# Kernel optimization log

Hardware: AMD Instinct MI355X
Metric: run time of the kernel (lower is better)

Reference implementation:

```python
import jax, jax.numpy as jnp
import numpy as np

N_STATE = 1024
N_HEAD = 16
HEAD_DIM = N_STATE // N_HEAD


def setup_inputs() -> dict:
    key = jax.random.key(0)
    ks = jax.random.split(key, 8)
    s = 0.02
    return {
        "x": jax.random.normal(ks[0], (4, 1500, N_STATE), dtype=jnp.float32),
        "Wq": jax.random.normal(ks[1], (N_STATE, N_STATE), dtype=jnp.float32) * s,
        "bq": jnp.zeros((N_STATE,), dtype=jnp.float32),
        "Wk": jax.random.normal(ks[2], (N_STATE, N_STATE), dtype=jnp.float32) * s,
        "Wv": jax.random.normal(ks[3], (N_STATE, N_STATE), dtype=jnp.float32) * s,
        "bv": jnp.zeros((N_STATE,), dtype=jnp.float32),
        "Wo": jax.random.normal(ks[4], (N_STATE, N_STATE), dtype=jnp.float32) * s,
        "bo": jnp.zeros((N_STATE,), dtype=jnp.float32),
    }


def reference(x, Wq, bq, Wk, Wv, bv, Wo, bo):
    B, S, _ = x.shape
    scale = HEAD_DIM ** (-0.5)
    # projections (torch Linear: y = x @ W.T + b)
    q = x @ Wq.T + bq
    k = x @ Wk.T
    v = x @ Wv.T + bv
    # [B, H, S, D]
    q = q.reshape(B, S, N_HEAD, HEAD_DIM).transpose(0, 2, 1, 3)
    k = k.reshape(B, S, N_HEAD, HEAD_DIM).transpose(0, 2, 1, 3)
    v = v.reshape(B, S, N_HEAD, HEAD_DIM).transpose(0, 2, 1, 3)
    # scores scaled AFTER the matmul, as in the original (qk * qk_scale)
    qk = jnp.einsum("bhqd,bhkd->bhqk", q, k) * scale
    w = jax.nn.softmax(qk, axis=-1)
    wv = jnp.einsum("bhqk,bhkd->bhqd", w, v)
    wv = wv.transpose(0, 2, 1, 3).reshape(B, S, N_STATE)
    return wv @ Wo.T + bo
```

## Files before the change

### kernel.cpp

```cpp
#include <hip/hip_runtime.h>
#include <hip/hip_bf16.h>
#include <stdint.h>

#define S_LEN  1500
#define S_PAD  1536
#define BATCH  4
#define NSTATE 1024
#define NHEAD  16
#define HDIM   64
#define MROWS  6000
#define C1     0.180336879f

typedef __attribute__((ext_vector_type(8)))  short short8;
typedef __attribute__((ext_vector_type(4)))  float floatx4;
typedef __attribute__((ext_vector_type(16))) float floatx16;

__device__ __forceinline__ unsigned short f2bf(float f) {
  union { float f; unsigned int u; } v; v.f = f;
  unsigned int r = v.u + 0x7fffu + ((v.u >> 16) & 1u);
  return (unsigned short)(r >> 16);
}

__device__ __forceinline__ void gld_lds16(const void* g, void* l) {
  __builtin_amdgcn_global_load_lds(
      (const __attribute__((address_space(1))) void*)g,
      (__attribute__((address_space(3))) void*)l, 16, 0, 0);
}

__global__ __launch_bounds__(256) void cvt_all(
    const float* __restrict__ x,  const float* __restrict__ Wq,
    const float* __restrict__ Wk, const float* __restrict__ Wv,
    const float* __restrict__ Wo, unsigned short* __restrict__ dst)
{
  const size_t NX = (size_t)MROWS * NSTATE;
  size_t e = ((size_t)blockIdx.x * 256 + threadIdx.x) * 4;
  const float* src; size_t off;
  if (e < NX) { src = x; off = e; }
  else {
    size_t t = e - NX;
    int wsel = (int)(t >> 20);
    off = t & ((1u << 20) - 1);
    src = (wsel == 0) ? Wq : (wsel == 1) ? Wk : (wsel == 2) ? Wv : Wo;
  }
  float4 v = *(const float4*)(src + off);
  uint2 o;
  o.x = (unsigned int)f2bf(v.x) | ((unsigned int)f2bf(v.y) << 16);
  o.y = (unsigned int)f2bf(v.z) | ((unsigned int)f2bf(v.w) << 16);
  *(uint2*)(dst + e) = o;
}

template <bool F32OUT>
__device__ __forceinline__ void gemm128_bt(
    const unsigned short* __restrict__ X,
    const unsigned short* __restrict__ W,
    const float* __restrict__ bias,
    void* __restrict__ Yv,
    int m0, int n0, float scale)
{
  __shared__ unsigned short As[2][128 * 32];
  __shared__ unsigned short Bs[2][128 * 32];

  const int tid  = threadIdx.x;
  const int lane = tid & 63;
  const int wid  = tid >> 6;
  const int wm   = (wid & 1) * 64;
  const int wn   = (wid >> 1) * 64;
  const int l15  = lane & 15;
  const int l4   = lane >> 4;

  floatx4 acc[4][4];
#pragma unroll
  for (int i = 0; i < 4; ++i)
#pragma unroll
    for (int j = 0; j < 4; ++j)
      acc[i][j] = (floatx4){0.f, 0.f, 0.f, 0.f};

  const int srow  = tid >> 2;
  const int scolb = (tid & 3) * 16;

  const char* xrp[2];
  const char* wrp[2];
#pragma unroll
  for (int r = 0; r < 2; ++r) {
    int arow = m0 + r * 64 + srow;
    if (arow > MROWS - 1) arow = MROWS - 1;
    xrp[r] = (const char*)X + (size_t)arow * NSTATE * 2 + scolb;
    int brow = n0 + r * 64 + srow;
    wrp[r] = (const char*)W + (size_t)brow * NSTATE * 2 + scolb;
  }

  for (int k0 = 0; k0 < NSTATE; k0 += 64) {
    __syncthreads();
#pragma unroll
    for (int h = 0; h < 2; ++h) {
      int kb = (k0 + h * 32) * 2;
#pragma unroll
      for (int r = 0; r < 2; ++r) {
        gld_lds16(xrp[r] + kb, (char*)As[h] + r * 4096 + wid * 1024);
        gld_lds16(wrp[r] + kb, (char*)Bs[h] + r * 4096 + wid * 1024);
      }
    }
    __syncthreads();

#pragma unroll
    for (int h = 0; h < 2; ++h) {
      short8 a[4], b[4];
#pragma unroll
      for (int i = 0; i < 4; ++i)
        a[i] = *(const short8*)(As[h] + (wm + i * 16 + l15) * 32 + l4 * 8);
#pragma unroll
      for (int j = 0; j < 4; ++j)
        b[j] = *(const short8*)(Bs[h] + (wn + j * 16 + l15) * 32 + l4 * 8);
#pragma unroll
      for (int i = 0; i < 4; ++i)
#pragma unroll
        for (int j = 0; j < 4; ++j)
          acc[i][j] = __builtin_amdgcn_mfma_f32_16x16x32_bf16(a[i], b[j], acc[i][j], 0, 0, 0);
    }
  }

#pragma unroll
  for (int j = 0; j < 4; ++j) {
    int ng = n0 + wn + j * 16 + l15;
    float bias_v = bias ? bias[ng] : 0.f;
#pragma unroll
    for (int i = 0; i < 4; ++i) {
      int mgb = m0 + wm + i * 16 + l4 * 4;
#pragma unroll
      for (int r = 0; r < 4; ++r) {
        int mg = mgb + r;
        if (mg < MROWS) {
          float val = (acc[i][j][r] + bias_v) * scale;
          if (F32OUT) ((float*)Yv)[(size_t)mg * NSTATE + ng] = val;
          else        ((unsigned short*)Yv)[(size_t)mg * NSTATE + ng] = f2bf(val);
        }
      }
    }
  }
}

__global__ __launch_bounds__(256) void proj_qkv(
    const unsigned short* __restrict__ X,
    const unsigned short* __restrict__ Wq, const unsigned short* __restrict__ Wk,
    const unsigned short* __restrict__ Wv,
    const float* __restrict__ bq, const float* __restrict__ bv,
    unsigned short* __restrict__ q, unsigned short* __restrict__ k,
    unsigned short* __restrict__ v)
{
  const int z = blockIdx.z;
  const unsigned short* W = (z == 0) ? Wq : (z == 1) ? Wk : Wv;
  const float* bias       = (z == 0) ? bq : (z == 1) ? (const float*)nullptr : bv;
  unsigned short* Y       = (z == 0) ? q  : (z == 1) ? k  : v;
  float scale             = (z == 0) ? C1 : 1.0f;
  gemm128_bt<false>(X, W, bias, Y, blockIdx.y * 128, blockIdx.x * 128, scale);
}

__global__ __launch_bounds__(256) void proj_o(
    const unsigned short* __restrict__ X, const unsigned short* __restrict__ W,
    const float* __restrict__ bias, float* __restrict__ Y)
{
  gemm128_bt<true>(X, W, bias, Y, blockIdx.y * 128, blockIdx.x * 128, 1.0f);
}

__global__ __launch_bounds__(256) void vtrans(
    const unsigned short* __restrict__ v, unsigned short* __restrict__ vt)
{
  __shared__ unsigned short T[64][72];
  const int tid = threadIdx.x;
  const int st = blockIdx.x * 64, h = blockIdx.y, b = blockIdx.z;
#pragma unroll
  for (int rr = 0; rr < 2; ++rr) {
    int sl = rr * 32 + (tid >> 3);
    int dl = (tid & 7) * 8;
    int s  = st + sl;
    uint4 val = make_uint4(0u, 0u, 0u, 0u);
    if (s < S_LEN)
      val = *(const uint4*)&v[((size_t)b * S_LEN + s) * NSTATE + h * HDIM + dl];
    *(uint4*)&T[sl][dl] = val;
  }
  __syncthreads();
#pragma unroll
  for (int rr = 0; rr < 2; ++rr) {
    int dl = rr * 32 + (tid >> 3);
    int s0 = (tid & 7) * 8;
    unsigned short tmp[8];
#pragma unroll
    for (int j2 = 0; j2 < 8; ++j2) tmp[j2] = T[s0 + j2][dl];
    *(uint4*)&vt[(((size_t)b * NHEAD + h) * HDIM + dl) * S_PAD + st + s0] =
        *(const uint4*)tmp;
  }
}

__global__ __launch_bounds__(256, 4) void attn32t(
    const unsigned short* __restrict__ Q, const unsigned short* __restrict__ K,
    const unsigned short* __restrict__ VT, unsigned short* __restrict__ O)
{
  __shared__ unsigned short SMEM[16384];
  unsigned short* Ks  = SMEM;
  unsigned short* Vts = SMEM + 8192;
  unsigned short* Os  = SMEM;

  const int tid  = threadIdx.x;
  const int lane = tid & 63;
  const int w    = tid >> 6;
  const int l31  = lane & 31;
  const int lhi  = lane >> 5;
  const int qt = blockIdx.x, h = blockIdx.y, b = blockIdx.z;
  const size_t base  = ((size_t)b * S_LEN) * NSTATE + h * HDIM;
  const size_t vbase = (((size_t)b * NHEAD + h) * HDIM) * S_PAD;

  short8 qf[4];
  {
    int qrow = qt * 128 + w * 32 + l31;
    if (qrow > S_LEN - 1) qrow = S_LEN - 1;
    const unsigned short* qp = Q + base + (size_t)qrow * NSTATE;
#pragma unroll
    for (int c = 0; c < 4; ++c)
      qf[c] = *(const short8*)(qp + c * 16 + lhi * 8);
  }

  short8 ones;
#pragma unroll
  for (int i = 0; i < 8; ++i) ones[i] = (short)0x3F80;

  floatx16 oacc[2], oacc_l;
  oacc[0] = (floatx16)(0.f);
  oacc[1] = (floatx16)(0.f);
  oacc_l  = (floatx16)(0.f);

  for (int t = 0; t < 12; ++t) {
    __syncthreads();
#pragma unroll
    for (int qq = 0; qq < 4; ++qq) {
      int row  = (w * 4 + qq) * 8 + (lane >> 3);
      int logc = (lane & 7) ^ (row & 7);
      int s = t * 128 + row; if (s > S_LEN - 1) s = S_LEN - 1;
      gld_lds16(&K[base + (size_t)s * NSTATE + logc * 8],
                (char*)Ks + (w * 4 + qq) * 1024);
    }
#pragma unroll
    for (int qq = 0; qq < 4; ++qq) {
      int d    = (w * 4 + qq) * 4 + (lane >> 4);
      int logc = (lane & 15) ^ (d & 7);
      gld_lds16(&VT[vbase + (size_t)d * S_PAD + t * 128 + logc * 8],
                (char*)Vts + (w * 4 + qq) * 1024);
    }
    __syncthreads();

#pragma unroll
    for (int kvt = 0; kvt < 4; ++kvt) {
      floatx16 sacc = (floatx16)(0.f);
#pragma unroll
      for (int c = 0; c < 4; ++c) {
        int row  = kvt * 32 + l31;
        int phys = (c * 2 + lhi) ^ (row & 7);
        short8 ak = *(const short8*)(Ks + row * 64 + phys * 8);
        sacc = __builtin_amdgcn_mfma_f32_32x32x16_bf16(ak, qf[c], sacc, 0, 0, 0);
      }

      if (t == 11 && kvt >= 2) {
        if (kvt == 3) {
#pragma unroll
          for (int r = 0; r < 16; ++r) sacc[r] = -3.0e38f;
        } else {
#pragma unroll
          for (int r = 12; r < 16; ++r) sacc[r] = lhi ? -3.0e38f : sacc[r];
        }
      }

      unsigned int pk[8], ex[8];
#pragma unroll
      for (int i = 0; i < 8; ++i) {
        float p0 = exp2f(sacc[2 * i]);
        float p1 = exp2f(sacc[2 * i + 1]);
        __hip_bfloat162 h2 = __float22bfloat162_rn(float2{p0, p1});
        unsigned int u;
        __builtin_memcpy(&u, &h2, 4);
        pk[i] = u;
      }
#pragma unroll
      for (int i = 0; i < 8; ++i)
        ex[i] = __shfl_xor((unsigned int)pk[i], 32, 64);

      int4 f0i, f1i;
      f0i.x = lhi ? ex[2] : pk[0];
      f0i.y = lhi ? ex[3] : pk[1];
      f0i.z = lhi ? pk[2] : ex[0];
      f0i.w = lhi ? pk[3] : ex[1];
      f1i.x = lhi ? ex[6] : pk[4];
      f1i.y = lhi ? ex[7] : pk[5];
      f1i.z = lhi ? pk[6] : ex[4];
      f1i.w = lhi ? pk[7] : ex[5];
      short8 f0 = *(short8*)&f0i;
      short8 f1 = *(short8*)&f1i;

      oacc_l = __builtin_amdgcn_mfma_f32_32x32x16_bf16(ones, f0, oacc_l, 0, 0, 0);
      oacc_l = __builtin_amdgcn_mfma_f32_32x32x16_bf16(ones, f1, oacc_l, 0, 0, 0);

#pragma unroll
      for (int dt = 0; dt < 2; ++dt) {
        int d = dt * 32 + l31;
        int p0 = ((kvt * 4 + 0) + lhi) ^ (d & 7);
        int p1 = ((kvt * 4 + 2) + lhi) ^ (d & 7);
        short8 av0 = *(const short8*)(Vts + d * 128 + p0 * 8);
        short8 av1 = *(const short8*)(Vts + d * 128 + p1 * 8);
        oacc[dt] = __builtin_amdgcn_mfma_f32_32x32x16_bf16(av0, f0, oacc[dt], 0, 0, 0);
        oacc[dt] = __builtin_amdgcn_mfma_f32_32x32x16_bf16(av1, f1, oacc[dt], 0, 0, 0);
      }
    }
  }

  float inv = 1.f / oacc_l[0];

  __syncthreads();
#pragma unroll
  for (int dt = 0; dt < 2; ++dt)
#pragma unroll
    for (int g = 0; g < 4; ++g) {
      int d0 = dt * 32 + g * 8 + lhi * 4;
      float v0 = oacc[dt][4 * g + 0] * inv;
      float v1 = oacc[dt][4 * g + 1] * inv;
      float v2 = oacc[dt][4 * g + 2] * inv;
      float v3 = oacc[dt][4 * g + 3] * inv;
      uint2 pk2;
      pk2.x = (unsigned int)f2bf(v0) | ((unsigned int)f2bf(v1) << 16);
      pk2.y = (unsigned int)f2bf(v2) | ((unsigned int)f2bf(v3) << 16);
      *(uint2*)&Os[(w * 32 + l31) * 72 + d0] = pk2;
    }
  __syncthreads();
#pragma unroll
  for (int pass = 0; pass < 4; ++pass) {
    int e = pass * 256 + tid;
    int row = e >> 3, ch = e & 7;
    int s = qt * 128 + row;
    if (s < S_LEN)
      *(uint4*)&O[base + (size_t)s * NSTATE + ch * 8] = *(const uint4*)&Os[row * 72 + ch * 8];
  }
}

extern "C" void kernel_launch(void* const* d_in, const int* in_sizes, int n_in,
                              void* d_out, int out_size, void* d_ws, size_t ws_size,
                              hipStream_t stream) {
  const float* x  = (const float*)d_in[0];
  const float* Wq = (const float*)d_in[1];
  const float* bq = (const float*)d_in[2];
  const float* Wk = (const float*)d_in[3];
  const float* Wv = (const float*)d_in[4];
  const float* bv = (const float*)d_in[5];
  const float* Wo = (const float*)d_in[6];
  const float* bo = (const float*)d_in[7];
  float* out = (float*)d_out;

  const size_t NX = (size_t)MROWS * NSTATE;
  const size_t NW = (size_t)NSTATE * NSTATE;

  unsigned short* xb  = (unsigned short*)d_ws;
  unsigned short* Wqb = xb  + NX;
  unsigned short* Wkb = Wqb + NW;
  unsigned short* Wvb = Wkb + NW;
  unsigned short* Wob = Wvb + NW;
  unsigned short* q   = Wob + NW;
  unsigned short* k   = q + NX;
  unsigned short* v   = k + NX;
  unsigned short* vt  = v + NX;
  unsigned short* wv  = xb;

  dim3 blk(256);
  const size_t n4_total = (NX + 4 * NW) / 4;
  cvt_all<<<dim3((int)(n4_total / 256)), blk, 0, stream>>>(x, Wq, Wk, Wv, Wo, xb);
  proj_qkv<<<dim3(8, 47, 3), blk, 0, stream>>>(xb, Wqb, Wkb, Wvb, bq, bv, q, k, v);
  vtrans<<<dim3(24, NHEAD, BATCH), blk, 0, stream>>>(v, vt);
  attn32t<<<dim3(12, NHEAD, BATCH), blk, 0, stream>>>(q, k, vt, wv);
  proj_o<<<dim3(8, 47, 1), blk, 0, stream>>>(wv, Wob, bo, out);
}
```

Before: 284.3 us.

## Fuse V transpose into V-projection epilogue and swap GEMM grid order

The V projection now writes its output directly in the transposed, padded per-head layout through a shared-memory staged epilogue, removing the separate vtrans kernel and the intermediate V buffer round trip. The GEMM grids are also reoriented so blockIdx.x walks M tiles, changing block rasterization and cache reuse of weights. The padded tail columns of vt are no longer zero-filled, and the new epilogue adds an extra sync and division-based index math.

```diff
diff --git a/kernel.cpp b/kernel.cpp
--- a/kernel.cpp
+++ b/kernel.cpp
@@ -49,7 +49,7 @@
   *(uint2*)(dst + e) = o;
 }
 
-template <bool F32OUT>
+template <int MODE>
 __device__ __forceinline__ void gemm128_bt(
     const unsigned short* __restrict__ X,
     const unsigned short* __restrict__ W,
@@ -57,8 +57,9 @@
     void* __restrict__ Yv,
     int m0, int n0, float scale)
 {
-  __shared__ unsigned short As[2][128 * 32];
-  __shared__ unsigned short Bs[2][128 * 32];
+  __shared__ unsigned short SM[17408];
+  unsigned short* Asp = SM;
+  unsigned short* Bsp = SM + 8192;
 
   const int tid  = threadIdx.x;
   const int lane = tid & 63;
@@ -96,21 +97,23 @@
       int kb = (k0 + h * 32) * 2;
 #pragma unroll
       for (int r = 0; r < 2; ++r) {
-        gld_lds16(xrp[r] + kb, (char*)As[h] + r * 4096 + wid * 1024);
-        gld_lds16(wrp[r] + kb, (char*)Bs[h] + r * 4096 + wid * 1024);
+        gld_lds16(xrp[r] + kb, (char*)SM + h * 8192 + r * 4096 + wid * 1024);
+        gld_lds16(wrp[r] + kb, (char*)SM + 16384 + h * 8192 + r * 4096 + wid * 1024);
       }
     }
     __syncthreads();
 
 #pragma unroll
     for (int h = 0; h < 2; ++h) {
+      const unsigned short* Ah = Asp + h * 4096;
+      const unsigned short* Bh = Bsp + h * 4096;
       short8 a[4], b[4];
 #pragma unroll
       for (int i = 0; i < 4; ++i)
-        a[i] = *(const short8*)(As[h] + (wm + i * 16 + l15) * 32 + l4 * 8);
+        a[i] = *(const short8*)(Ah + (wm + i * 16 + l15) * 32 + l4 * 8);
 #pragma unroll
       for (int j = 0; j < 4; ++j)
-        b[j] = *(const short8*)(Bs[h] + (wn + j * 16 + l15) * 32 + l4 * 8);
+        b[j] = *(const short8*)(Bh + (wn + j * 16 + l15) * 32 + l4 * 8);
 #pragma unroll
       for (int i = 0; i < 4; ++i)
 #pragma unroll
@@ -119,20 +122,64 @@
     }
   }
 
-#pragma unroll
-  for (int j = 0; j < 4; ++j) {
-    int ng = n0 + wn + j * 16 + l15;
-    float bias_v = bias ? bias[ng] : 0.f;
-#pragma unroll
-    for (int i = 0; i < 4; ++i) {
-      int mgb = m0 + wm + i * 16 + l4 * 4;
-#pragma unroll
-      for (int r = 0; r < 4; ++r) {
-        int mg = mgb + r;
-        if (mg < MROWS) {
-          float val = (acc[i][j][r] + bias_v) * scale;
-          if (F32OUT) ((float*)Yv)[(size_t)mg * NSTATE + ng] = val;
-          else        ((unsigned short*)Yv)[(size_t)mg * NSTATE + ng] = f2bf(val);
+  if (MODE != 2) {
+#pragma unroll
+    for (int j = 0; j < 4; ++j) {
+      int ng = n0 + wn + j * 16 + l15;
+      float bias_v = bias ? bias[ng] : 0.f;
+#pragma unroll
+      for (int i = 0; i < 4; ++i) {
+        int mgb = m0 + wm + i * 16 + l4 * 4;
+#pragma unroll
+        for (int r = 0; r < 4; ++r) {
+          int mg = mgb + r;
+          if (mg < MROWS) {
+            float val = (acc[i][j][r] + bias_v) * scale;
+            if (MODE == 1) ((float*)Yv)[(size_t)mg * NSTATE + ng] = val;
+            else           ((unsigned short*)Yv)[(size_t)mg * NSTATE + ng] = f2bf(val);
+          }
+        }
+      }
+    }
+  } else {
+    unsigned short* vt = (unsigned short*)Yv;
+    __syncthreads();
+#pragma unroll
+    for (int j = 0; j < 4; ++j) {
+      int nl = wn + j * 16 + l15;
+      float bias_v = bias[n0 + nl];
+#pragma unroll
+      for (int i = 0; i < 4; ++i) {
+        int mlb = wm + i * 16 + l4 * 4;
+#pragma unroll
+        for (int r = 0; r < 4; ++r)
+          SM[nl * 136 + mlb + r] = f2bf(acc[i][j][r] + bias_v);
+      }
+    }
+    __syncthreads();
+#pragma unroll
+    for (int pass = 0; pass < 8; ++pass) {
+      int e   = pass * 256 + tid;
+      int nl  = e >> 4;
+      int m0l = (e & 15) * 8;
+      int ng  = n0 + nl;
+      int hh  = ng >> 6, dd = ng & 63;
+      int mg  = m0 + m0l;
+      int b1  = mg / 1500;
+      int s1  = mg - b1 * 1500;
+      if (mg + 7 < MROWS && s1 + 7 < S_LEN) {
+        *(uint4*)&vt[(((size_t)b1 * NHEAD + hh) * HDIM + dd) * S_PAD + s1] =
+            *(const uint4*)&SM[nl * 136 + m0l];
+      } else {
+#pragma unroll
+        for (int jj = 0; jj < 8; ++jj) {
+          int m = mg + jj;
+          if (m < MROWS) {
+            int b2 = m / 1500;
+            int s2 = m - b2 * 1500;
+            vt[(((size_t)b2 * NHEAD + hh) * HDIM + dd) * S_PAD + s2] =
+                SM[nl * 136 + m0l + jj];
+          }
         }
       }
     }
@@ -145,50 +192,20 @@
     const unsigned short* __restrict__ Wv,
     const float* __restrict__ bq, const float* __restrict__ bv,
     unsigned short* __restrict__ q, unsigned short* __restrict__ k,
-    unsigned short* __restrict__ v)
+    unsigned short* __restrict__ vt)
 {
   const int z = blockIdx.z;
-  const unsigned short* W = (z == 0) ? Wq : (z == 1) ? Wk : Wv;
-  const float* bias       = (z == 0) ? bq : (z == 1) ? (const float*)nullptr : bv;
-  unsigned short* Y       = (z == 0) ? q  : (z == 1) ? k  : v;
-  float scale             = (z == 0) ? C1 : 1.0f;
-  gemm128_bt<false>(X, W, bias, Y, blockIdx.y * 128, blockIdx.x * 128, scale);
+  const int m0 = blockIdx.x * 128, n0 = blockIdx.y * 128;
+  if (z == 0)      gemm128_bt<0>(X, Wq, bq,      q,  m0, n0, C1);
+  else if (z == 1) gemm128_bt<0>(X, Wk, nullptr, k,  m0, n0, 1.0f);
+  else             gemm128_bt<2>(X, Wv, bv,      vt, m0, n0, 1.0f);
 }
 
 __global__ __launch_bounds__(256) void proj_o(
     const unsigned short* __restrict__ X, const unsigned short* __restrict__ W,
     const float* __restrict__ bias, float* __restrict__ Y)
 {
-  gemm128_bt<true>(X, W, bias, Y, blockIdx.y * 128, blockIdx.x * 128, 1.0f);
-}
-
-__global__ __launch_bounds__(256) void vtrans(
-    const unsigned short* __restrict__ v, unsigned short* __restrict__ vt)
-{
-  __shared__ unsigned short T[64][72];
-  const int tid = threadIdx.x;
-  const int st = blockIdx.x * 64, h = blockIdx.y, b = blockIdx.z;
-#pragma unroll
-  for (int rr = 0; rr < 2; ++rr) {
-    int sl = rr * 32 + (tid >> 3);
-    int dl = (tid & 7) * 8;
-    int s  = st + sl;
-    uint4 val = make_uint4(0u, 0u, 0u, 0u);
-    if (s < S_LEN)
-      val = *(const uint4*)&v[((size_t)b * S_LEN + s) * NSTATE + h * HDIM + dl];
-    *(uint4*)&T[sl][dl] = val;
-  }
-  __syncthreads();
-#pragma unroll
-  for (int rr = 0; rr < 2; ++rr) {
-    int dl = rr * 32 + (tid >> 3);
-    int s0 = (tid & 7) * 8;
-    unsigned short tmp[8];
-#pragma unroll
-    for (int j2 = 0; j2 < 8; ++j2) tmp[j2] = T[s0 + j2][dl];
-    *(uint4*)&vt[(((size_t)b * NHEAD + h) * HDIM + dl) * S_PAD + st + s0] =
-        *(const uint4*)tmp;
-  }
+  gemm128_bt<1>(X, W, bias, Y, blockIdx.x * 128, blockIdx.y * 128, 1.0f);
 }
 
 __global__ __launch_bounds__(256, 4) void attn32t(
@@ -361,15 +378,13 @@
   unsigned short* Wob = Wvb + NW;
   unsigned short* q   = Wob + NW;
   unsigned short* k   = q + NX;
-  unsigned short* v   = k + NX;
-  unsigned short* vt  = v + NX;
+  unsigned short* vt  = k + NX;
   unsigned short* wv  = xb;
 
   dim3 blk(256);
   const size_t n4_total = (NX + 4 * NW) / 4;
   cvt_all<<<dim3((int)(n4_total / 256)), blk, 0, stream>>>(x, Wq, Wk, Wv, Wo, xb);
-  proj_qkv<<<dim3(8, 47, 3), blk, 0, stream>>>(xb, Wqb, Wkb, Wvb, bq, bv, q, k, v);
-  vtrans<<<dim3(24, NHEAD, BATCH), blk, 0, stream>>>(v, vt);
+  proj_qkv<<<dim3(47, 8, 3), blk, 0, stream>>>(xb, Wqb, Wkb, Wvb, bq, bv, q, k, vt);
   attn32t<<<dim3(12, NHEAD, BATCH), blk, 0, stream>>>(q, k, vt, wv);
-  proj_o<<<dim3(8, 47, 1), blk, 0, stream>>>(wv, Wob, bo, out);
-}
+  proj_o<<<dim3(47, 8, 1), blk, 0, stream>>>(wv, Wob, bo, out);
+}
```

Result: faster. 269.6 us (-5.2%).
